# Kernel optimization log

Measured on AMD Instinct MI355X. Metric: run time of the kernel, lower is better.

## Reference

```python
import jax, jax.numpy as jnp
import numpy as np

V, D, H, L, FF, T, B, W = 32000, 1024, 16, 8, 4096, 1024, 2, 256
HALF = FF // 2
HD = D // H
EPS = 1e-5


def layer_norm(x, g, b):
    mu = jnp.mean(x, axis=-1, keepdims=True)
    var = jnp.mean(jnp.square(x - mu), axis=-1, keepdims=True)
    return (x - mu) * jax.lax.rsqrt(var + EPS) * g + b


def setup_inputs() -> dict:
    key = jax.random.key(0)
    ks = jax.random.split(key, 12)
    s = 0.02
    nrm = lambda k, shape: jax.random.normal(k, shape, jnp.float32) * s
    idx = jax.random.randint(ks[0], (B, T), 0, V, dtype=jnp.int64)
    return {
        "idx": idx,
        "tok_emb": nrm(ks[1], (V, D)),
        "pos_emb": nrm(ks[2], (T, D)),
        "ln1_g": jnp.ones((L, D), jnp.float32),
        "ln1_b": jnp.zeros((L, D), jnp.float32),
        "qkv_w": nrm(ks[3], (L, 3 * D, D)),
        "out_w": nrm(ks[4], (L, D, D)),
        "ln2_g": jnp.ones((L, D), jnp.float32),
        "ln2_b": jnp.zeros((L, D), jnp.float32),
        "a_w1": nrm(ks[5], (L, HALF, D)),
        "a_w2": nrm(ks[6], (L, D, HALF)),
        "f_w1": nrm(ks[7], (L, HALF, D)),
        "f_w2": nrm(ks[8], (L, D, HALF)),
        "lnf_g": jnp.ones((D,), jnp.float32),
        "lnf_b": jnp.zeros((D,), jnp.float32),
        "head_w": nrm(ks[9], (V, D)),
    }


def _forward(idx, tok_emb, pos_emb, ln1_g, ln1_b, qkv_w, out_w, ln2_g, ln2_b,
             a_w1, a_w2, f_w1, f_w2, lnf_g, lnf_b, head_w):
    Bc, Tc = idx.shape
    x = tok_emb[idx] + pos_emb[:Tc]  # [B,T,D]
    # sliding-window causal band: attend to j in [i-W+1, i]
    i = jnp.arange(Tc)
    d = i[:, None] - i[None, :]
    mask = jnp.where((d >= 0) & (d < W), 0.0, -jnp.inf).astype(x.dtype)  # [T,T]
    scale = 1.0 / np.sqrt(HD)

    def block(x, p):
        l1g, l1b, qw, ow, l2g, l2b, aw1, aw2, fw1, fw2 = p
        h = layer_norm(x, l1g, l1b)
        qkv = (h @ qw.T).reshape(Bc, Tc, 3, H, HD)
        q, k, v = qkv[:, :, 0], qkv[:, :, 1], qkv[:, :, 2]  # [B,T,H,HD]
        attn = jnp.einsum('bqhd,bkhd->bhqk', q, k) * scale + mask
        attn = jax.nn.softmax(attn, axis=-1)
        o = jnp.einsum('bhqk,bkhd->bqhd', attn, v).reshape(Bc, Tc, D)
        x = x + o @ ow.T
        h2 = layer_norm(x, l2g, l2b)
        mlp = (jax.nn.gelu(h2 @ aw1.T, approximate=False) @ aw2.T
               + jax.nn.gelu(h2 @ fw1.T, approximate=False) @ fw2.T)
        return x + mlp, None

    x, _ = jax.lax.scan(block, x, (ln1_g, ln1_b, qkv_w, out_w, ln2_g, ln2_b,
                                   a_w1, a_w2, f_w1, f_w2))
    return layer_norm(x, lnf_g, lnf_b) @ head_w.T  # [B,T,V]


def reference(idx, tok_emb, pos_emb, ln1_g, ln1_b, qkv_w, out_w, ln2_g, ln2_b,
              a_w1, a_w2, f_w1, f_w2, lnf_g, lnf_b, head_w):
    return _forward(idx, tok_emb, pos_emb, ln1_g, ln1_b, qkv_w, out_w,
                    ln2_g, ln2_b, a_w1, a_w2, f_w1, f_w2, lnf_g, lnf_b, head_w)
```

## Files before the change

### kernel.cpp

```cpp
#include <hip/hip_runtime.h>

typedef __bf16 bf16x8 __attribute__((ext_vector_type(8)));
typedef __bf16 bf16x4 __attribute__((ext_vector_type(4)));
typedef float  f32x4  __attribute__((ext_vector_type(4)));
typedef unsigned int u32x4 __attribute__((ext_vector_type(4)));

#define MFMA16(a, b, c) __builtin_amdgcn_mfma_f32_16x16x32_bf16(a, b, c, 0, 0, 0)

__device__ __forceinline__ void gload_lds16(const void* g, void* l) {
  __builtin_amdgcn_global_load_lds(
      (const __attribute__((address_space(1))) void*)g,
      (__attribute__((address_space(3))) void*)l, 16, 0, 0);
}

__device__ __forceinline__ void waitvm(int vm) {
  if (vm == 6)      asm volatile("s_waitcnt vmcnt(6)" ::: "memory");
  else if (vm == 4) asm volatile("s_waitcnt vmcnt(4)" ::: "memory");
  else if (vm == 3) asm volatile("s_waitcnt vmcnt(3)" ::: "memory");
  else              asm volatile("s_waitcnt vmcnt(0)" ::: "memory");
}

__global__ __launch_bounds__(256) void cvt_kernel(
    const float* __restrict__ s, __bf16* __restrict__ d, int n8) {
  int i = blockIdx.x * 256 + threadIdx.x;
  if (i >= n8) return;
  size_t o = (size_t)i * 8;
  f32x4 a = *(const f32x4*)(s + o), b = *(const f32x4*)(s + o + 4);
  bf16x8 v;
  v[0] = (__bf16)a[0]; v[1] = (__bf16)a[1]; v[2] = (__bf16)a[2]; v[3] = (__bf16)a[3];
  v[4] = (__bf16)b[0]; v[5] = (__bf16)b[1]; v[6] = (__bf16)b[2]; v[7] = (__bf16)b[3];
  *(bf16x8*)(d + o) = v;
}

__global__ __launch_bounds__(256) void cat_w1_kernel(
    const float* __restrict__ a, const float* __restrict__ f, __bf16* __restrict__ d) {
  int i = blockIdx.x * 256 + threadIdx.x;
  int k = (i & 127) * 8;
  int r = i >> 7;
  const float* s = (r < 2048) ? a + ((size_t)r << 10) + k
                              : f + ((size_t)(r - 2048) << 10) + k;
  f32x4 va = *(const f32x4*)s, vb = *(const f32x4*)(s + 4);
  bf16x8 v;
  v[0] = (__bf16)va[0]; v[1] = (__bf16)va[1]; v[2] = (__bf16)va[2]; v[3] = (__bf16)va[3];
  v[4] = (__bf16)vb[0]; v[5] = (__bf16)vb[1]; v[6] = (__bf16)vb[2]; v[7] = (__bf16)vb[3];
  *(bf16x8*)(d + ((size_t)i << 3)) = v;
}

__global__ __launch_bounds__(256) void cat_w2_kernel(
    const float* __restrict__ a, const float* __restrict__ f, __bf16* __restrict__ d) {
  int i = blockIdx.x * 256 + threadIdx.x;
  int k = (i & 511) * 8;
  int r = i >> 9;
  const float* s = (k < 2048) ? a + (size_t)r * 2048 + k
                              : f + (size_t)r * 2048 + (k - 2048);
  f32x4 va = *(const f32x4*)s, vb = *(const f32x4*)(s + 4);
  bf16x8 v;
  v[0] = (__bf16)va[0]; v[1] = (__bf16)va[1]; v[2] = (__bf16)va[2]; v[3] = (__bf16)va[3];
  v[4] = (__bf16)vb[0]; v[5] = (__bf16)vb[1]; v[6] = (__bf16)vb[2]; v[7] = (__bf16)vb[3];
  *(bf16x8*)(d + ((size_t)i << 3)) = v;
}

__global__ __launch_bounds__(256) void embed_kernel(
    const int* __restrict__ idx, const float* __restrict__ te,
    const float* __restrict__ pe, float* __restrict__ x) {
  int m = blockIdx.x;
  int t = m & 1023;
  int tok = idx[m];
  int c = threadIdx.x * 4;
  f32x4 a = *(const f32x4*)(te + (size_t)tok * 1024 + c);
  f32x4 p = *(const f32x4*)(pe + (size_t)t * 1024 + c);
  *(f32x4*)(x + (size_t)m * 1024 + c) = a + p;
}

__global__ __launch_bounds__(256) void ln_kernel(
    const float* __restrict__ x, const float* __restrict__ g,
    const float* __restrict__ bb, __bf16* __restrict__ out) {
  int row = blockIdx.x, tid = threadIdx.x;
  int wid = tid >> 6, lane = tid & 63;
  f32x4 v = *(const f32x4*)(x + (size_t)row * 1024 + tid * 4);
  float s = v[0] + v[1] + v[2] + v[3];
  #pragma unroll
  for (int off = 32; off >= 1; off >>= 1) s += __shfl_xor(s, off);
  __shared__ float red1[4], red2[4];
  if (lane == 0) red1[wid] = s;
  __syncthreads();
  float mu = (red1[0] + red1[1] + red1[2] + red1[3]) * (1.0f / 1024.0f);
  float d0 = v[0] - mu, d1 = v[1] - mu, d2 = v[2] - mu, d3 = v[3] - mu;
  float q = d0 * d0 + d1 * d1 + d2 * d2 + d3 * d3;
  #pragma unroll
  for (int off = 32; off >= 1; off >>= 1) q += __shfl_xor(q, off);
  if (lane == 0) red2[wid] = q;
  __syncthreads();
  float var = (red2[0] + red2[1] + red2[2] + red2[3]) * (1.0f / 1024.0f);
  float inv = rsqrtf(var + 1e-5f);
  f32x4 gg = *(const f32x4*)(g + tid * 4);
  f32x4 bv = *(const f32x4*)(bb + tid * 4);
  bf16x4 o4;
  o4[0] = (__bf16)(d0 * inv * gg[0] + bv[0]);
  o4[1] = (__bf16)(d1 * inv * gg[1] + bv[1]);
  o4[2] = (__bf16)(d2 * inv * gg[2] + bv[2]);
  o4[3] = (__bf16)(d3 * inv * gg[3] + bv[3]);
  *(bf16x4*)(out + (size_t)row * 1024 + tid * 4) = o4;
}

template <int EPI>
__global__ __launch_bounds__(512, 2) void gemm256(
    const __bf16* __restrict__ A, int lda,
    const __bf16* __restrict__ B, int ldb, int K,
    float* __restrict__ Cf, __bf16* __restrict__ Cb, int ldc, int nbx) {
  __shared__ __align__(16) __bf16 lds[49152];
  const int tid = threadIdx.x, lane = tid & 63, w = tid >> 6;
  const int l15 = lane & 15, l4 = lane >> 4;
  const int wr = w >> 2, wc = w & 3;

  int nwg = gridDim.x, id = blockIdx.x;
  int q = nwg >> 3, r = nwg & 7;
  int xcd = id & 7, pos = id >> 3;
  int nid = (xcd < r ? xcd * (q + 1) : r * (q + 1) + (xcd - r) * q) + pos;
  int row0 = (nid % nbx) * 256, col0 = (nid / nbx) * 256;

  const __bf16* ag = A + (size_t)row0 * lda;
  const __bf16* bg = B + (size_t)col0 * ldb;

  f32x4 acc[8][4];
  #pragma unroll
  for (int i = 0; i < 8; ++i)
    #pragma unroll
    for (int j = 0; j < 4; ++j) acc[i][j] = (f32x4){0.f, 0.f, 0.f, 0.f};

  int srow[2], scol[2];
  #pragma unroll
  for (int i = 0; i < 2; ++i) {
    int p = (w + i * 8) * 1024 + lane * 16;
    int row = p >> 6, ch = (p >> 4) & 3;
    srow[i] = row;
    scol[i] = (ch ^ ((row >> 1) & 3)) * 8;
  }
  const int fx = (((l4 << 4) ^ (((l15 >> 1) & 3) << 4)) >> 1);

  auto stageA = [&](int t, int c) {
    #pragma unroll
    for (int i = 0; i < 2; ++i)
      gload_lds16(ag + (size_t)srow[i] * lda + t * 32 + scol[i],
                  &lds[c * 16384 + (w + i * 8) * 512]);
  };
  auto stageB = [&](int t, int c) {
    #pragma unroll
    for (int i = 0; i < 2; ++i)
      gload_lds16(bg + (size_t)srow[i] * ldb + t * 32 + scol[i],
                  &lds[c * 16384 + 8192 + (w + i * 8) * 512]);
  };

  auto kgroup = [&](int t2, int c, int cn, int vm, bool stg) {
    if (stg) stageA(t2, cn);
    waitvm(vm);
    __builtin_amdgcn_sched_barrier(0);
    __builtin_amdgcn_s_barrier();
    __builtin_amdgcn_sched_barrier(0);
    const int cb = c * 16384;
    bf16x8 bfr[4], af[4];
    #pragma unroll
    for (int ni = 0; ni < 4; ++ni)
      bfr[ni] = *(const bf16x8*)&lds[cb + 8192 + (wc * 64 + ni * 16 + l15) * 32 + fx];
    #pragma unroll
    for (int mi = 0; mi < 4; ++mi)
      af[mi] = *(const bf16x8*)&lds[cb + (wr * 128 + mi * 16 + l15) * 32 + fx];
    __builtin_amdgcn_s_setprio(1);
    #pragma unroll
    for (int mi = 0; mi < 4; ++mi)
      #pragma unroll
      for (int ni = 0; ni < 4; ++ni)
        acc[mi][ni] = MFMA16(af[mi], bfr[ni], acc[mi][ni]);
    __builtin_amdgcn_s_setprio(0);
    #pragma unroll
    for (int mi = 0; mi < 4; ++mi)
      af[mi] = *(const bf16x8*)&lds[cb + (wr * 128 + (mi + 4) * 16 + l15) * 32 + fx];
    if (stg) stageB(t2, cn);
    __builtin_amdgcn_s_setprio(1);
    #pragma unroll
    for (int mi = 0; mi < 4; ++mi)
      #pragma unroll
      for (int ni = 0; ni < 4; ++ni)
        acc[mi + 4][ni] = MFMA16(af[mi], bfr[ni], acc[mi + 4][ni]);
    __builtin_amdgcn_s_setprio(0);
    __builtin_amdgcn_sched_barrier(0);
    __builtin_amdgcn_s_barrier();
    __builtin_amdgcn_sched_barrier(0);
  };

  const int NT = K >> 5;
  stageA(0, 0); stageB(0, 0);
  stageA(1, 1); stageB(1, 1);

  int c = 0;
  for (int t = 0; t < NT - 2; ++t) {
    int cn = c + 2; if (cn >= 3) cn -= 3;
    kgroup(t + 2, c, cn, 6, true);
    c = (c == 2) ? 0 : c + 1;
  }
  kgroup(0, c, 0, 4, false);
  c = (c == 2) ? 0 : c + 1;
  kgroup(0, c, 0, 0, false);

  #pragma unroll
  for (int mi = 0; mi < 8; ++mi)
    #pragma unroll
    for (int ni = 0; ni < 4; ++ni)
      #pragma unroll
      for (int rr = 0; rr < 4; ++rr) {
        int row = row0 + wr * 128 + mi * 16 + l4 * 4 + rr;
        int col = col0 + wc * 64 + ni * 16 + l15;
        float v = acc[mi][ni][rr];
        size_t off = (size_t)row * ldc + col;
        if (EPI == 0) {
          Cf[off] = v;
        } else if (EPI == 1) {
          Cb[off] = (__bf16)v;
        } else {
          float gv = 0.5f * v * (1.0f + erff(v * 0.70710678118654752f));
          Cb[off] = (__bf16)gv;
        }
      }
}

template <int BN, int EPI>
__global__ __launch_bounds__(256) void gemm_bf16(
    const __bf16* __restrict__ A, int lda,
    const __bf16* __restrict__ B, int ldb, int K,
    float* __restrict__ Cf, __bf16* __restrict__ Cb, int ldc,
    const float* __restrict__ resid, int nbx) {
  constexpr int ACCN = BN / 32;
  constexpr int LB = BN / 64;
  constexpr int L = 2 + LB;
  __shared__ __align__(16) __bf16 As[2 * 4096];
  __shared__ __align__(16) __bf16 Bs[2 * BN * 32];

  int nwg = gridDim.x, id = blockIdx.x;
  int q = nwg >> 3, r = nwg & 7;
  int xcd = id & 7, pos = id >> 3;
  int nid = (xcd < r ? xcd * (q + 1) : r * (q + 1) + (xcd - r) * q) + pos;
  int row0 = (nid % nbx) * 128;
  int col0 = (nid / nbx) * BN;

  const int tid = threadIdx.x, lane = tid & 63, wid = tid >> 6;
  const int l15 = lane & 15, l4 = lane >> 4;
  const int wr = wid >> 1, wc = wid & 1;
  const int fx = (((l4 << 4) ^ (((l15 >> 1) & 3) << 4)) >> 1);

  f32x4 acc[4][ACCN];
  #pragma unroll
  for (int i = 0; i < 4; ++i)
    #pragma unroll
    for (int j = 0; j < ACCN; ++j) acc[i][j] = (f32x4){0.f, 0.f, 0.f, 0.f};

  const __bf16* aptr = A + (size_t)row0 * lda;
  const __bf16* bptr = B + (size_t)col0 * ldb;

  auto stage = [&](int t, int p) {
    #pragma unroll
    for (int i = 0; i < 2; ++i) {
      int ch = tid + 256 * i;
      int rr = ch >> 2, kc = ch & 3;
      gload_lds16(aptr + (size_t)rr * lda + t * 32 + (kc ^ ((rr >> 1) & 3)) * 8,
                  &As[p * 4096 + ch * 8]);
    }
    #pragma unroll
    for (int i = 0; i < LB; ++i) {
      int ch = tid + 256 * i;
      int rr = ch >> 2, kc = ch & 3;
      gload_lds16(bptr + (size_t)rr * ldb + t * 32 + (kc ^ ((rr >> 1) & 3)) * 8,
                  &Bs[p * BN * 32 + ch * 8]);
    }
  };

  const int NT = K >> 5;
  stage(0, 0);
  for (int t = 0; t < NT; ++t) {
    int p = t & 1;
    bool stg = (t + 1 < NT);
    if (stg) stage(t + 1, p ^ 1);
    waitvm(stg ? L : 0);
    __builtin_amdgcn_sched_barrier(0);
    __builtin_amdgcn_s_barrier();
    __builtin_amdgcn_sched_barrier(0);
    bf16x8 af[4], bfr[ACCN];
    #pragma unroll
    for (int mi = 0; mi < 4; ++mi)
      af[mi] = *(const bf16x8*)&As[p * 4096 + (wr * 64 + mi * 16 + l15) * 32 + fx];
    #pragma unroll
    for (int ni = 0; ni < ACCN; ++ni)
      bfr[ni] = *(const bf16x8*)&Bs[p * BN * 32 + (wc * (BN / 2) + ni * 16 + l15) * 32 + fx];
    #pragma unroll
    for (int mi = 0; mi < 4; ++mi)
      #pragma unroll
      for (int ni = 0; ni < ACCN; ++ni)
        acc[mi][ni] = MFMA16(af[mi], bfr[ni], acc[mi][ni]);
    __builtin_amdgcn_sched_barrier(0);
    __builtin_amdgcn_s_barrier();
    __builtin_amdgcn_sched_barrier(0);
  }

  #pragma unroll
  for (int mi = 0; mi < 4; ++mi)
    #pragma unroll
    for (int ni = 0; ni < ACCN; ++ni)
      #pragma unroll
      for (int rr = 0; rr < 4; ++rr) {
        int row = row0 + wr * 64 + mi * 16 + l4 * 4 + rr;
        int col = col0 + wc * (BN / 2) + ni * 16 + l15;
        float v = acc[mi][ni][rr];
        size_t off = (size_t)row * ldc + col;
        if (EPI == 0) {
          Cf[off] = v;
        } else if (EPI == 1) {
          Cb[off] = (__bf16)v;
        } else if (EPI == 2) {
          float gv = 0.5f * v * (1.0f + erff(v * 0.70710678118654752f));
          Cb[off] = (__bf16)gv;
        } else {
          Cf[off] = resid[off] + v;
        }
      }
}

__global__ __launch_bounds__(256) void attn_kernel(
    const __bf16* __restrict__ qkv, __bf16* __restrict__ o) {
  const int bid = blockIdx.x;
  const int qt = bid & 15, h = (bid >> 4) & 15, b = bid >> 8;
  const int qs = qt * 64;
  const int ntiles = (qt + 1 < 5) ? (qt + 1) : 5;
  const int kt0 = qt - (ntiles - 1);

  __shared__ __align__(16) __bf16 Qs[64][72];
  __shared__ __align__(16) __bf16 KVs[64][72];
  __shared__ __align__(16) __bf16 Ssm[64][328];
  __shared__ float rsum[64];

  const int tid = threadIdx.x;
  const int lane = tid & 63, wid = tid >> 6;
  const int l15 = lane & 15, l4 = lane >> 4;
  const size_t rs = 3072;
  const __bf16* qbase = qkv + ((size_t)(b * 1024 + qs)) * rs + h * 64;

  #pragma unroll
  for (int i = 0; i < 2; ++i) {
    int c = tid * 2 + i;
    int rr = c >> 3, dc = c & 7;
    *(u32x4*)&Qs[rr][dc * 8] = *(const u32x4*)(qbase + (size_t)rr * rs + dc * 8);
  }

  for (int it = 0; it < ntiles; ++it) {
    int kt = kt0 + it;
    const __bf16* kbase = qkv + ((size_t)(b * 1024 + kt * 64)) * rs + 1024 + h * 64;
    __syncthreads();
    #pragma unroll
    for (int i = 0; i < 2; ++i) {
      int c = tid * 2 + i;
      int rr = c >> 3, dc = c & 7;
      *(u32x4*)&KVs[rr][dc * 8] = *(const u32x4*)(kbase + (size_t)rr * rs + dc * 8);
    }
    __syncthreads();
    bf16x8 aq[2];
    #pragma unroll
    for (int kk = 0; kk < 2; ++kk)
      aq[kk] = *(const bf16x8*)&Qs[16 * wid + l15][kk * 32 + l4 * 8];
    #pragma unroll
    for (int n = 0; n < 4; ++n) {
      f32x4 c4 = (f32x4){0.f, 0.f, 0.f, 0.f};
      #pragma unroll
      for (int kk = 0; kk < 2; ++kk) {
        bf16x8 bk = *(const bf16x8*)&KVs[n * 16 + l15][kk * 32 + l4 * 8];
        c4 = MFMA16(aq[kk], bk, c4);
      }
      int kj = kt * 64 + n * 16 + l15;
      int colS = it * 64 + n * 16 + l15;
      #pragma unroll
      for (int rr = 0; rr < 4; ++rr) {
        int qi = qs + 16 * wid + l4 * 4 + rr;
        int d = qi - kj;
        float sv = c4[rr] * 0.125f;
        Ssm[16 * wid + l4 * 4 + rr][colS] =
            (d >= 0 && d < 256) ? (__bf16)sv : (__bf16)(-1e30f);
      }
    }
  }

  for (int rr = 0; rr < 16; ++rr) {
    int row = 16 * wid + rr;
    float vals[5];
    #pragma unroll
    for (int i = 0; i < 5; ++i) vals[i] = -3e38f;
    #pragma unroll
    for (int i = 0; i < 5; ++i)
      if (i < ntiles) vals[i] = (float)Ssm[row][lane + 64 * i];
    float m = vals[0];
    #pragma unroll
    for (int i = 1; i < 5; ++i) m = fmaxf(m, vals[i]);
    #pragma unroll
    for (int off = 32; off >= 1; off >>= 1) m = fmaxf(m, __shfl_xor(m, off));
    float s = 0.f;
    #pragma unroll
    for (int i = 0; i < 5; ++i)
      if (i < ntiles) {
        float p = __expf(vals[i] - m);
        s += p;
        Ssm[row][lane + 64 * i] = (__bf16)p;
      }
    #pragma unroll
    for (int off = 32; off >= 1; off >>= 1) s += __shfl_xor(s, off);
    if (lane == 0) rsum[row] = s;
  }

  f32x4 oacc[4];
  #pragma unroll
  for (int n = 0; n < 4; ++n) oacc[n] = (f32x4){0.f, 0.f, 0.f, 0.f};

  for (int it = 0; it < ntiles; ++it) {
    int kt = kt0 + it;
    const __bf16* vbase = qkv + ((size_t)(b * 1024 + kt * 64)) * rs + 2048 + h * 64;
    __syncthreads();
    if (tid < 64) {
      int k0 = (tid >> 3) * 8, d0 = (tid & 7) * 8;
      bf16x8 vr[8];
      #pragma unroll
      for (int rr = 0; rr < 8; ++rr)
        vr[rr] = *(const bf16x8*)(vbase + (size_t)(k0 + rr) * rs + d0);
      #pragma unroll
      for (int j = 0; j < 8; ++j) {
        bf16x8 w;
        #pragma unroll
        for (int rr = 0; rr < 8; ++rr) w[rr] = vr[rr][j];
        *(bf16x8*)&KVs[d0 + j][k0] = w;
      }
    }
    __syncthreads();
    #pragma unroll
    for (int kk = 0; kk < 2; ++kk) {
      bf16x8 ap = *(const bf16x8*)&Ssm[16 * wid + l15][it * 64 + kk * 32 + l4 * 8];
      #pragma unroll
      for (int n = 0; n < 4; ++n) {
        bf16x8 bv = *(const bf16x8*)&KVs[n * 16 + l15][kk * 32 + l4 * 8];
        oacc[n] = MFMA16(ap, bv, oacc[n]);
      }
    }
  }

  #pragma unroll
  for (int n = 0; n < 4; ++n)
    #pragma unroll
    for (int rr = 0; rr < 4; ++rr) {
      int qrow = 16 * wid + l4 * 4 + rr;
      float inv = 1.0f / rsum[qrow];
      size_t m = (size_t)(b * 1024 + qs + qrow);
      o[m * 1024 + h * 64 + n * 16 + l15] = (__bf16)(oacc[n][rr] * inv);
    }
}

extern "C" void kernel_launch(void* const* d_in, const int* in_sizes, int n_in,
                              void* d_out, int out_size, void* d_ws, size_t ws_size,
                              hipStream_t stream) {
  (void)in_sizes; (void)n_in; (void)out_size;
  const int*   idx     = (const int*)d_in[0];
  const float* tok_emb = (const float*)d_in[1];
  const float* pos_emb = (const float*)d_in[2];
  const float* ln1_g   = (const float*)d_in[3];
  const float* ln1_b   = (const float*)d_in[4];
  const float* qkv_w   = (const float*)d_in[5];
  const float* out_w   = (const float*)d_in[6];
  const float* ln2_g   = (const float*)d_in[7];
  const float* ln2_b   = (const float*)d_in[8];
  const float* a_w1    = (const float*)d_in[9];
  const float* a_w2    = (const float*)d_in[10];
  const float* f_w1    = (const float*)d_in[11];
  const float* f_w2    = (const float*)d_in[12];
  const float* lnf_g   = (const float*)d_in[13];
  const float* lnf_b   = (const float*)d_in[14];
  const float* head_w  = (const float*)d_in[15];
  float* out = (float*)d_out;

  char* ws = (char*)d_ws;
  float*  x    = (float*)(ws);
  __bf16* h    = (__bf16*)(ws + 8388608);
  __bf16* qkv  = (__bf16*)(ws + 12582912);
  __bf16* oatt = (__bf16*)(ws + 25165824);
  __bf16* gcat = (__bf16*)(ws + 29360128);

  const bool full = ws_size >= 313000000ull;

  __bf16 *wq, *wo, *w1c, *w2c, *wh;
  if (full) {
    wq  = (__bf16*)(ws + 46137344);
    wo  = (__bf16*)(ws + 96468992);
    w1c = (__bf16*)(ws + 113246208);
    w2c = (__bf16*)(ws + 180355072);
    wh  = (__bf16*)(ws + 247463936);
    cvt_kernel<<<12288, 256, 0, stream>>>(qkv_w, wq, 3145728);
    cvt_kernel<<<4096, 256, 0, stream>>>(out_w, wo, 1048576);
    for (int l = 0; l < 8; ++l) {
      cat_w1_kernel<<<2048, 256, 0, stream>>>(
          a_w1 + (size_t)l * 2048 * 1024, f_w1 + (size_t)l * 2048 * 1024,
          w1c + (size_t)l * 4096 * 1024);
      cat_w2_kernel<<<2048, 256, 0, stream>>>(
          a_w2 + (size_t)l * 1024 * 2048, f_w2 + (size_t)l * 1024 * 2048,
          w2c + (size_t)l * 1024 * 4096);
    }
    cvt_kernel<<<16000, 256, 0, stream>>>(head_w, wh, 4096000);
  } else {
    wq  = (__bf16*)(ws + 46137344);
    wo  = (__bf16*)(ws + 52428800);
    w1c = (__bf16*)(ws + 54525952);
    w2c = (__bf16*)(ws + 62914560);
    wh  = (__bf16*)(ws + 46137344);
  }

  embed_kernel<<<2048, 256, 0, stream>>>(idx, tok_emb, pos_emb, x);

  for (int l = 0; l < 8; ++l) {
    const __bf16 *wq_l, *wo_l, *w1_l, *w2_l;
    if (full) {
      wq_l = wq + (size_t)l * 3072 * 1024;
      wo_l = wo + (size_t)l * 1024 * 1024;
      w1_l = w1c + (size_t)l * 4096 * 1024;
      w2_l = w2c + (size_t)l * 1024 * 4096;
    } else {
      cvt_kernel<<<1536, 256, 0, stream>>>(qkv_w + (size_t)l * 3072 * 1024, wq, 393216);
      cvt_kernel<<<512, 256, 0, stream>>>(out_w + (size_t)l * 1024 * 1024, wo, 131072);
      cat_w1_kernel<<<2048, 256, 0, stream>>>(
          a_w1 + (size_t)l * 2048 * 1024, f_w1 + (size_t)l * 2048 * 1024, w1c);
      cat_w2_kernel<<<2048, 256, 0, stream>>>(
          a_w2 + (size_t)l * 1024 * 2048, f_w2 + (size_t)l * 1024 * 2048, w2c);
      wq_l = wq; wo_l = wo; w1_l = w1c; w2_l = w2c;
    }

    ln_kernel<<<2048, 256, 0, stream>>>(x, ln1_g + l * 1024, ln1_b + l * 1024, h);
    gemm256<1><<<8 * 12, 512, 0, stream>>>(
        h, 1024, wq_l, 1024, 1024, nullptr, qkv, 3072, 8);
    attn_kernel<<<512, 256, 0, stream>>>(qkv, oatt);
    gemm_bf16<64, 3><<<16 * 16, 256, 0, stream>>>(
        oatt, 1024, wo_l, 1024, 1024, x, nullptr, 1024, x, 16);
    ln_kernel<<<2048, 256, 0, stream>>>(x, ln2_g + l * 1024, ln2_b + l * 1024, h);
    gemm256<2><<<8 * 16, 512, 0, stream>>>(
        h, 1024, w1_l, 1024, 1024, nullptr, gcat, 4096, 8);
    gemm_bf16<64, 3><<<16 * 16, 256, 0, stream>>>(
        gcat, 4096, w2_l, 4096, 4096, x, nullptr, 1024, x, 16);
  }

  if (!full) {
    cvt_kernel<<<16000, 256, 0, stream>>>(head_w, wh, 4096000);
  }
  ln_kernel<<<2048, 256, 0, stream>>>(x, lnf_g, lnf_b, h);
  gemm256<0><<<8 * 125, 512, 0, stream>>>(
      h, 1024, wh, 1024, 1024, out, nullptr, 32000, 8);
}
```

Measured before the change: 2.082 ms.

## Restructure GEMM main loop to BK=64 double-buffer with interleaved quarter stages

The 256x256 GEMM now uses a K-tile of 64 with two LDS buffers instead of three 32-wide buffers. Each iteration is split into four MFMA quadrants, and the global-to-LDS loads for the next tile are spread between them with barriers and an 8-way XOR swizzle. Occupancy drops to one block per CU to make room for the larger LDS footprint. Separately, the attention V-transpose staging now uses all threads with 4x4 chunks instead of 64 threads with 8x8 chunks. The aim is fewer barriers per unit of K and better load/compute overlap, at the cost of lower occupancy and extra barriers within each iteration.

Result: slower. 2.199 ms (+5.6%).

```diff
diff --git a/kernel.cpp b/kernel.cpp
--- a/kernel.cpp
+++ b/kernel.cpp
@@ -17,6 +17,7 @@
   if (vm == 6)      asm volatile("s_waitcnt vmcnt(6)" ::: "memory");
   else if (vm == 4) asm volatile("s_waitcnt vmcnt(4)" ::: "memory");
   else if (vm == 3) asm volatile("s_waitcnt vmcnt(3)" ::: "memory");
+  else if (vm == 2) asm volatile("s_waitcnt vmcnt(2)" ::: "memory");
   else              asm volatile("s_waitcnt vmcnt(0)" ::: "memory");
 }
 
@@ -104,11 +105,11 @@
 }
 
 template <int EPI>
-__global__ __launch_bounds__(512, 2) void gemm256(
+__global__ __launch_bounds__(512, 1) void gemm256(
     const __bf16* __restrict__ A, int lda,
     const __bf16* __restrict__ B, int ldb, int K,
     float* __restrict__ Cf, __bf16* __restrict__ Cb, int ldc, int nbx) {
-  __shared__ __align__(16) __bf16 lds[49152];
+  __shared__ __align__(16) __bf16 lds[65536];
   const int tid = threadIdx.x, lane = tid & 63, w = tid >> 6;
   const int l15 = lane & 15, l4 = lane >> 4;
   const int wr = w >> 2, wc = w & 3;
@@ -128,79 +129,95 @@
     #pragma unroll
     for (int j = 0; j < 4; ++j) acc[i][j] = (f32x4){0.f, 0.f, 0.f, 0.f};
 
-  int srow[2], scol[2];
-  #pragma unroll
-  for (int i = 0; i < 2; ++i) {
-    int p = (w + i * 8) * 1024 + lane * 16;
-    int row = p >> 6, ch = (p >> 4) & 3;
-    srow[i] = row;
-    scol[i] = (ch ^ ((row >> 1) & 3)) * 8;
-  }
-  const int fx = (((l4 << 4) ^ (((l15 >> 1) & 3) << 4)) >> 1);
-
-  auto stageA = [&](int t, int c) {
-    #pragma unroll
-    for (int i = 0; i < 2; ++i)
-      gload_lds16(ag + (size_t)srow[i] * lda + t * 32 + scol[i],
-                  &lds[c * 16384 + (w + i * 8) * 512]);
+  int srow[2], scol[2], sdst[2];
+  #pragma unroll
+  for (int j = 0; j < 2; ++j) {
+    int p = (w * 2 + j) * 1024 + lane * 16;
+    int row = p >> 7, ch = (p >> 4) & 7;
+    srow[j] = row;
+    scol[j] = (ch ^ (row & 7)) << 3;
+    sdst[j] = (w * 2 + j) * 512 + lane * 8;
+  }
+  auto stageHalf = [&](int t, int hf, int d) {
+    const __bf16* src = (hf < 2) ? ag : bg;
+    int ld = (hf < 2) ? lda : ldb;
+    int base = ((hf < 2) ? 0 : 32768) + d * 16384 + (hf & 1) * 8192;
+    int grow = (hf & 1) * 128;
+    #pragma unroll
+    for (int j = 0; j < 2; ++j)
+      gload_lds16(src + (size_t)(grow + srow[j]) * ld + t * 64 + scol[j],
+                  &lds[base + sdst[j]]);
   };
-  auto stageB = [&](int t, int c) {
-    #pragma unroll
-    for (int i = 0; i < 2; ++i)
-      gload_lds16(bg + (size_t)srow[i] * ldb + t * 32 + scol[i],
-                  &lds[c * 16384 + 8192 + (w + i * 8) * 512]);
+
+  const int akey = l15 & 7;
+  auto ldA = [&](int d, int mi, int kk) -> bf16x8 {
+    return *(const bf16x8*)&lds[d * 16384 + (wr * 128 + mi * 16 + l15) * 64 +
+                                (((kk * 4 + l4) ^ akey) << 3)];
   };
-
-  auto kgroup = [&](int t2, int c, int cn, int vm, bool stg) {
-    if (stg) stageA(t2, cn);
-    waitvm(vm);
-    __builtin_amdgcn_sched_barrier(0);
-    __builtin_amdgcn_s_barrier();
-    __builtin_amdgcn_sched_barrier(0);
-    const int cb = c * 16384;
-    bf16x8 bfr[4], af[4];
-    #pragma unroll
-    for (int ni = 0; ni < 4; ++ni)
-      bfr[ni] = *(const bf16x8*)&lds[cb + 8192 + (wc * 64 + ni * 16 + l15) * 32 + fx];
+  auto ldB = [&](int d, int ni, int kk) -> bf16x8 {
+    return *(const bf16x8*)&lds[32768 + d * 16384 + (wc * 64 + ni * 16 + l15) * 64 +
+                                (((kk * 4 + l4) ^ akey) << 3)];
+  };
+
+  bf16x8 af[4][2], bf[4][2];
+
+  auto mfma_quad = [&](int mi0, int ni0, const bf16x8 a[4][2]) {
+    __builtin_amdgcn_s_setprio(1);
     #pragma unroll
     for (int mi = 0; mi < 4; ++mi)
-      af[mi] = *(const bf16x8*)&lds[cb + (wr * 128 + mi * 16 + l15) * 32 + fx];
-    __builtin_amdgcn_s_setprio(1);
-    #pragma unroll
-    for (int mi = 0; mi < 4; ++mi)
-      #pragma unroll
-      for (int ni = 0; ni < 4; ++ni)
-        acc[mi][ni] = MFMA16(af[mi], bfr[ni], acc[mi][ni]);
+      #pragma unroll
+      for (int ni = 0; ni < 2; ++ni)
+        #pragma unroll
+        for (int kk = 0; kk < 2; ++kk)
+          acc[mi0 + mi][ni0 + ni] = MFMA16(a[mi][kk], bf[ni0 + ni][kk], acc[mi0 + mi][ni0 + ni]);
     __builtin_amdgcn_s_setprio(0);
-    #pragma unroll
-    for (int mi = 0; mi < 4; ++mi)
-      af[mi] = *(const bf16x8*)&lds[cb + (wr * 128 + (mi + 4) * 16 + l15) * 32 + fx];
-    if (stg) stageB(t2, cn);
-    __builtin_amdgcn_s_setprio(1);
-    #pragma unroll
-    for (int mi = 0; mi < 4; ++mi)
-      #pragma unroll
-      for (int ni = 0; ni < 4; ++ni)
-        acc[mi + 4][ni] = MFMA16(af[mi], bfr[ni], acc[mi + 4][ni]);
-    __builtin_amdgcn_s_setprio(0);
+  };
+  auto bar = [&]() {
     __builtin_amdgcn_sched_barrier(0);
     __builtin_amdgcn_s_barrier();
     __builtin_amdgcn_sched_barrier(0);
   };
 
-  const int NT = K >> 5;
-  stageA(0, 0); stageB(0, 0);
-  stageA(1, 1); stageB(1, 1);
-
-  int c = 0;
-  for (int t = 0; t < NT - 2; ++t) {
-    int cn = c + 2; if (cn >= 3) cn -= 3;
-    kgroup(t + 2, c, cn, 6, true);
-    c = (c == 2) ? 0 : c + 1;
-  }
-  kgroup(0, c, 0, 4, false);
-  c = (c == 2) ? 0 : c + 1;
-  kgroup(0, c, 0, 0, false);
+  const int NT = K >> 6;
+  stageHalf(0, 0, 0); stageHalf(0, 1, 0); stageHalf(0, 2, 0); stageHalf(0, 3, 0);
+
+  for (int t = 0; t < NT; ++t) {
+    const int d = t & 1;
+    const bool stg = (t + 1 < NT);
+    if (stg) stageHalf(t + 1, 0, d ^ 1);
+    waitvm(stg ? 2 : 0);
+    bar();
+    #pragma unroll
+    for (int mi = 0; mi < 4; ++mi)
+      #pragma unroll
+      for (int kk = 0; kk < 2; ++kk) af[mi][kk] = ldA(d, mi, kk);
+    #pragma unroll
+    for (int ni = 0; ni < 2; ++ni)
+      #pragma unroll
+      for (int kk = 0; kk < 2; ++kk) bf[ni][kk] = ldB(d, ni, kk);
+    mfma_quad(0, 0, af);
+    bar();
+    #pragma unroll
+    for (int ni = 2; ni < 4; ++ni)
+      #pragma unroll
+      for (int kk = 0; kk < 2; ++kk) bf[ni][kk] = ldB(d, ni, kk);
+    if (stg) stageHalf(t + 1, 1, d ^ 1);
+    bar();
+    mfma_quad(0, 2, af);
+    bar();
+    #pragma unroll
+    for (int mi = 0; mi < 4; ++mi)
+      #pragma unroll
+      for (int kk = 0; kk < 2; ++kk) af[mi][kk] = ldA(d, mi + 4, kk);
+    if (stg) stageHalf(t + 1, 2, d ^ 1);
+    bar();
+    mfma_quad(4, 2, af);
+    bar();
+    if (stg) stageHalf(t + 1, 3, d ^ 1);
+    bar();
+    mfma_quad(4, 0, af);
+    bar();
+  }
 
   #pragma unroll
   for (int mi = 0; mi < 8; ++mi)
@@ -419,18 +436,18 @@
     int kt = kt0 + it;
     const __bf16* vbase = qkv + ((size_t)(b * 1024 + kt * 64)) * rs + 2048 + h * 64;
     __syncthreads();
-    if (tid < 64) {
-      int k0 = (tid >> 3) * 8, d0 = (tid & 7) * 8;
-      bf16x8 vr[8];
-      #pragma unroll
-      for (int rr = 0; rr < 8; ++rr)
-        vr[rr] = *(const bf16x8*)(vbase + (size_t)(k0 + rr) * rs + d0);
-      #pragma unroll
-      for (int j = 0; j < 8; ++j) {
-        bf16x8 w;
+    {
+      int k0 = (tid >> 4) * 4, d0 = (tid & 15) * 4;
+      bf16x4 vr[4];
+      #pragma unroll
+      for (int rr = 0; rr < 4; ++rr)
+        vr[rr] = *(const bf16x4*)(vbase + (size_t)(k0 + rr) * rs + d0);
+      #pragma unroll
+      for (int j = 0; j < 4; ++j) {
+        bf16x4 wv;
         #pragma unroll
-        for (int rr = 0; rr < 8; ++rr) w[rr] = vr[rr][j];
-        *(bf16x8*)&KVs[d0 + j][k0] = w;
+        for (int rr = 0; rr < 4; ++rr) wv[rr] = vr[rr][j];
+        *(bf16x4*)&KVs[d0 + j][k0] = wv;
       }
     }
     __syncthreads();
```
